# Kernel tuning notes

Hardware: AMD Instinct MI355X
Metric: run time of the kernel (lower is better)

## Reference

```python
import jax, jax.numpy as jnp
import numpy as np

# ---- SLAYER neuron / simulation params (network.yaml equivalents) ----
THETA = 10.0       # spiking threshold
TAU_SR = 10.0      # synaptic (PSP) alpha-kernel time constant
TAU_REF = 1.0      # refractory alpha-kernel time constant
SCALE_REF = 2.0
TS = 1.0           # simulation step
T_SAMPLE = 350     # number of timesteps

B, NIN, NHID, NOUT = 32, 2312, 512, 10


def _alpha_kernel(tau, mult=1.0, eps=0.01):
    # mirrors slayer._calculateAlphaKernel truncation rule
    ks = []
    for t in np.arange(0.0, T_SAMPLE, TS):
        v = mult * t / tau * np.exp(1.0 - t / tau)
        if abs(v) < eps and t > tau:
            break
        ks.append(v)
    return jnp.asarray(np.asarray(ks, dtype=np.float32))

SRM_KERNEL = _alpha_kernel(TAU_SR)                        # truncated PSP kernel
D_REF = float(np.exp(-TS / TAU_REF))                      # geometric decay of refractory alpha kernel
C_REF = float(-SCALE_REF * THETA * np.e * TS / TAU_REF)   # refKernel[j] = C_REF * j * D_REF**j


def psp(x):
    # causal temporal conv with the SRM alpha kernel, scaled by Ts. x: (B, C, T)
    b, c, t = x.shape
    k = SRM_KERNEL.shape[0]
    out = jax.lax.conv_general_dilated(
        x.reshape(b * c, 1, t), SRM_KERNEL[::-1].reshape(1, 1, k),
        window_strides=(1,), padding=[(k - 1, 0)])
    return (out * TS).reshape(b, c, t)


def spike(u_psp):
    # Sequential thresholding with FULL refractory recurrence: a spike at time s
    # adds refKernel[n-s] = C_REF*(n-s)*D_REF**(n-s) to all future potentials.
    # The alpha kernel is realized EXACTLY by a 2-state linear recurrence (x, y):
    #   x[n] = sum_s spk[s] * d^(n-s),  y[n] = sum_s spk[s] * (n-s) * d^(n-s)
    def step(carry, p_t):
        x, y = carry
        y = D_REF * (y + x)
        u = p_t + C_REF * y           # membrane potential after refractory response
        spk = (u >= THETA).astype(p_t.dtype)
        x = D_REF * x + spk
        return (x, y), spk / TS       # SLAYER emits spikes of magnitude 1/Ts
    b, c, _ = u_psp.shape
    init = (jnp.zeros((b, c), u_psp.dtype), jnp.zeros((b, c), u_psp.dtype))
    _, s = jax.lax.scan(step, init, jnp.moveaxis(u_psp, -1, 0))
    return jnp.moveaxis(s, 0, -1)


def setup_inputs() -> dict:
    key = jax.random.key(0)
    k1, k2, k3 = jax.random.split(key, 3)
    spikeInput = (jax.random.uniform(k1, (B, NIN, T_SAMPLE)) < 0.03).astype(jnp.float32) / TS
    W1 = jax.random.normal(k2, (NHID, NIN), jnp.float32) * 0.05
    W2 = jax.random.normal(k3, (NOUT, NHID), jnp.float32) * 0.5
    return {"spikeInput": spikeInput, "W1": W1, "W2": W2}


def reference(spikeInput, W1, W2):
    # fc (1x1x1 conv == per-timestep matmul) -> psp -> spike, twice
    s1 = spike(psp(jnp.einsum('oi,bit->bot', W1, spikeInput)))
    s2 = spike(psp(jnp.einsum('oi,bit->bot', W2, s1)))
    return s2
```

## Files before the change

### kernel.cpp

```cpp
#include <hip/hip_runtime.h>
#include <hip/hip_bf16.h>
#include <math.h>

#define B_    32
#define NIN_  2312
#define NHID_ 512
#define NOUT_ 10
#define T_    350
#define KLEN  77
#define MW    40
#define MAXA2 320

__global__ __launch_bounds__(256) void w1t_k(const float* __restrict__ W,
                                             float* __restrict__ WT) {
  __shared__ float tile[32][33];
  int i0 = blockIdx.x * 32, o0 = blockIdx.y * 32;
  int tx = threadIdx.x, tyb = threadIdx.y;
#pragma unroll
  for (int s = 0; s < 4; ++s) {
    int ty = tyb + s * 8;
    int o = o0 + ty, i = i0 + tx;
    if (i < NIN_) tile[ty][tx] = W[(size_t)o * NIN_ + i];
  }
  __syncthreads();
#pragma unroll
  for (int s = 0; s < 4; ++s) {
    int ty = tyb + s * 8;
    int i = i0 + ty, o = o0 + tx;
    if (i < NIN_) WT[(size_t)i * NHID_ + o] = tile[tx][ty];
  }
}

__global__ __launch_bounds__(256) void inmask_k(const float* __restrict__ X,
                                                unsigned long long* __restrict__ msk) {
  int wave = blockIdx.x * 4 + (threadIdx.x >> 6);
  int lane = threadIdx.x & 63;
  if (wave >= B_ * NIN_) return;
  int b = wave / NIN_, i = wave - b * NIN_;
  const float2* row = (const float2*)(X + (size_t)wave * T_);
  const unsigned long long bit = 1ull << (i & 63);
  unsigned long long* mb = msk + (size_t)b * T_ * MW + (i >> 6);
  for (int p = lane; p < T_ / 2; p += 64) {
    float2 v = row[p];
    if (v.x != 0.f) atomicOr(&mb[(size_t)(2 * p) * MW], bit);
    if (v.y != 0.f) atomicOr(&mb[(size_t)(2 * p + 1) * MW], bit);
  }
}

__global__ __launch_bounds__(256) void accum1_k(const unsigned long long* __restrict__ msk,
                                                const float* __restrict__ WT,
                                                float* __restrict__ Z1) {
  __shared__ unsigned short list[MAXA2];
  __shared__ int ntot;
  int bt = blockIdx.x, tid = threadIdx.x;
  if (tid < 64) {
    unsigned long long w = (tid < 37) ? msk[(size_t)bt * MW + tid] : 0ull;
    int pc = __popcll(w);
    int pre = pc;
#pragma unroll
    for (int d = 1; d < 64; d <<= 1) {
      int o = __shfl_up(pre, d);
      if (tid >= d) pre += o;
    }
    int base = pre - pc;
    if (tid == 63) ntot = pre;
    while (w) {
      int j = __builtin_ctzll(w);
      if (base < MAXA2) list[base] = (unsigned short)(tid * 64 + j);
      ++base;
      w &= w - 1;
    }
  }
  __syncthreads();
  int n = ntot;
  if (n > MAXA2) n = MAXA2;
  float a0 = 0.f, a1 = 0.f;
#pragma unroll 4
  for (int j = 0; j < n; ++j) {
    const float2* w2 = (const float2*)(WT + (size_t)list[j] * NHID_);
    float2 v = w2[tid];
    a0 += v.x;
    a1 += v.y;
  }
  float2* zr = (float2*)(Z1 + (size_t)bt * NHID_);
  zr[tid] = make_float2(a0, a1);
}

__global__ __launch_bounds__(64) void scan1_k(const float* __restrict__ Z1,
                                              unsigned long long* __restrict__ mask) {
  int lane = threadIdx.x;
  int b = blockIdx.x >> 3, g = blockIdx.x & 7;
  int h = g * 64 + lane;
  const double dp   = exp(-0.1);
  const double Ap   = exp(1.0) / 10.0;
  const double D77  = exp(-7.7);
  const float  Dref = (float)exp(-1.0);
  const float  Cref = (float)(-20.0 * exp(1.0));
  double Xc = 0.0, Yc = 0.0, Xd = 0.0, Yd = 0.0;
  float xr = 0.f, yr = 0.f;
  const float* zb = Z1 + (size_t)b * T_ * NHID_ + h;
  unsigned long long* mb = mask + (size_t)b * T_ * 8 + g;
  for (int t0 = 0; t0 < T_; t0 += 16) {
    float z[16], zd[16];
#pragma unroll
    for (int k = 0; k < 16; ++k) {
      int t = t0 + k;
      z[k]  = (t < T_) ? zb[(size_t)t * NHID_] : 0.f;
      zd[k] = (t >= KLEN && t < T_) ? zb[(size_t)(t - KLEN) * NHID_] : 0.f;
    }
#pragma unroll
    for (int k = 0; k < 16; ++k) {
      int t = t0 + k;
      if (t >= T_) break;
      Yc = dp * (Yc + Xc); Xc = dp * Xc + (double)z[k];
      Yd = dp * (Yd + Xd); Xd = dp * Xd + (double)zd[k];
      float p = (float)(Ap * (Yc - D77 * (Yd + 77.0 * Xd)));
      yr = Dref * (yr + xr);
      float u = p + Cref * yr;
      float s = (u >= 10.0f) ? 1.0f : 0.0f;
      xr = Dref * xr + s;
      unsigned long long bw = __ballot(u >= 10.0f);
      if (lane == 0) mb[(size_t)t * 8] = bw;
    }
  }
}

__global__ __launch_bounds__(256) void z2_k(const unsigned long long* __restrict__ mask,
                                            const float* __restrict__ W2,
                                            float* __restrict__ Z2) {
  int wave = blockIdx.x * 4 + (threadIdx.x >> 6);
  int lane = threadIdx.x & 63;
  if (wave >= B_ * T_) return;
  int b = wave / T_, t = wave - b * T_;
  const unsigned long long* m = mask + (size_t)wave * 8;
  if (lane < NOUT_) {
    const float* wr = W2 + (size_t)lane * NHID_;
    float acc = 0.f;
#pragma unroll
    for (int w = 0; w < 8; ++w) {
      unsigned long long mm = m[w];
      while (mm) {
        int j = __builtin_ctzll(mm);
        mm &= mm - 1;
        acc += wr[w * 64 + j];
      }
    }
    Z2[((size_t)b * NOUT_ + lane) * T_ + t] = acc;
  }
}

__global__ __launch_bounds__(64) void scan2_k(const float* __restrict__ Z2,
                                              float* __restrict__ out) {
  int n = blockIdx.x * 64 + threadIdx.x;
  if (n >= B_ * NOUT_) return;
  const double dp   = exp(-0.1);
  const double Ap   = exp(1.0) / 10.0;
  const double D77  = exp(-7.7);
  const float  Dref = (float)exp(-1.0);
  const float  Cref = (float)(-20.0 * exp(1.0));
  double Xc = 0.0, Yc = 0.0, Xd = 0.0, Yd = 0.0;
  float xr = 0.f, yr = 0.f;
  const float* row = Z2 + (size_t)n * T_;
  float* orow = out + (size_t)n * T_;
  float zc = row[0];
  float zdc = 0.f;
  for (int t = 0; t < T_; ++t) {
    float zn  = (t + 1 < T_) ? row[t + 1] : 0.f;
    float zdn = (t + 1 >= KLEN && t + 1 < T_) ? row[t + 1 - KLEN] : 0.f;
    Yc = dp * (Yc + Xc); Xc = dp * Xc + (double)zc;
    Yd = dp * (Yd + Xd); Xd = dp * Xd + (double)zdc;
    float p = (float)(Ap * (Yc - D77 * (Yd + 77.0 * Xd)));
    yr = Dref * (yr + xr);
    float u = p + Cref * yr;
    float s = (u >= 10.0f) ? 1.0f : 0.0f;
    xr = Dref * xr + s;
    orow[t] = s;
    zc = zn; zdc = zdn;
  }
}

extern "C" void kernel_launch(void* const* d_in, const int* in_sizes, int n_in,
                              void* d_out, int out_size, void* d_ws, size_t ws_size,
                              hipStream_t stream) {
  const float* X  = (const float*)d_in[0];
  const float* W1 = (const float*)d_in[1];
  const float* W2 = (const float*)d_in[2];
  float* out = (float*)d_out;

  char* ws = (char*)d_ws;
  size_t off = 0;
  float* W1T = (float*)(ws + off);                 off += (size_t)NIN_ * NHID_ * 4;
  unsigned long long* msk = (unsigned long long*)(ws + off); off += (size_t)B_ * T_ * MW * 8;
  float* Z1 = (float*)(ws + off);                  off += (size_t)B_ * T_ * NHID_ * 4;
  unsigned long long* mask = (unsigned long long*)(ws + off); off += (size_t)B_ * T_ * 8 * 8;
  float* Z2 = (float*)(ws + off);                  off += (size_t)B_ * NOUT_ * T_ * 4;
  if (off > ws_size) return;

  hipMemsetAsync(msk, 0, (size_t)B_ * T_ * MW * 8, stream);

  w1t_k<<<dim3((NIN_ + 31) / 32, NHID_ / 32), dim3(32, 8), 0, stream>>>(W1, W1T);
  inmask_k<<<(B_ * NIN_ + 3) / 4, 256, 0, stream>>>(X, msk);
  accum1_k<<<B_ * T_, 256, 0, stream>>>(msk, W1T, Z1);
  scan1_k<<<B_ * 8, 64, 0, stream>>>(Z1, mask);
  z2_k<<<(B_ * T_ + 3) / 4, 256, 0, stream>>>(mask, W2, Z2);
  scan2_k<<<(B_ * NOUT_ + 63) / 64, 64, 0, stream>>>(Z2, out);
}
```

Baseline: 416.9 us.

## Build input spike masks with ballots, split accumulation over output chunks

The input-mask kernel now assigns each wave a 64-input by 16-timestep tile and builds mask words with ballots and plain stores. This removes the atomicOr traffic and the memset of the mask buffer. The weight accumulation kernel is split into four 64-thread blocks per (batch, time), each covering a 128-column slice, which adds parallelism but recomputes the active-input list in each of the four blocks. The second scan now prefetches its inputs in chunks of 16 timesteps, as the first scan already does.

```diff
diff --git a/kernel.cpp b/kernel.cpp
--- a/kernel.cpp
+++ b/kernel.cpp
@@ -9,6 +9,8 @@
 #define T_    350
 #define KLEN  77
 #define MW    40
+#define NIB   37
+#define NTC   22
 #define MAXA2 320
 
 __global__ __launch_bounds__(256) void w1t_k(const float* __restrict__ W,
@@ -33,57 +35,70 @@
 
 __global__ __launch_bounds__(256) void inmask_k(const float* __restrict__ X,
                                                 unsigned long long* __restrict__ msk) {
-  int wave = blockIdx.x * 4 + (threadIdx.x >> 6);
+  int w = blockIdx.x * 4 + (threadIdx.x >> 6);
   int lane = threadIdx.x & 63;
-  if (wave >= B_ * NIN_) return;
-  int b = wave / NIN_, i = wave - b * NIN_;
-  const float2* row = (const float2*)(X + (size_t)wave * T_);
-  const unsigned long long bit = 1ull << (i & 63);
-  unsigned long long* mb = msk + (size_t)b * T_ * MW + (i >> 6);
-  for (int p = lane; p < T_ / 2; p += 64) {
-    float2 v = row[p];
-    if (v.x != 0.f) atomicOr(&mb[(size_t)(2 * p) * MW], bit);
-    if (v.y != 0.f) atomicOr(&mb[(size_t)(2 * p + 1) * MW], bit);
-  }
-}
-
-__global__ __launch_bounds__(256) void accum1_k(const unsigned long long* __restrict__ msk,
-                                                const float* __restrict__ WT,
-                                                float* __restrict__ Z1) {
+  if (w >= B_ * NIB * NTC) return;
+  int b = w / (NIB * NTC);
+  int rem = w - b * (NIB * NTC);
+  int iblk = rem / NTC, tc = rem - iblk * NTC;
+  int i = iblk * 64 + lane;
+  int t0 = tc * 16;
+  int nk = (t0 + 16 <= T_) ? 16 : (T_ - t0);
+  bool valid = (i < NIN_);
+  const float2* rp = (const float2*)(X + ((size_t)b * NIN_ + (valid ? i : 0)) * T_ + t0);
+  float2 v[8];
+#pragma unroll
+  for (int q = 0; q < 8; ++q) v[q] = make_float2(0.f, 0.f);
+  if (valid) {
+    int nw = nk >> 1;
+    for (int q = 0; q < nw; ++q) v[q] = rp[q];
+  }
+  unsigned long long* mrow = msk + ((size_t)b * T_ + t0) * MW + iblk;
+#pragma unroll
+  for (int k = 0; k < 16; ++k) {
+    if (k >= nk) break;
+    float xv = (k & 1) ? v[k >> 1].y : v[k >> 1].x;
+    unsigned long long bw = __ballot(xv != 0.0f);
+    if (lane == k) mrow[(size_t)k * MW] = bw;
+  }
+}
+
+__global__ __launch_bounds__(64) void accum1_k(const unsigned long long* __restrict__ msk,
+                                               const float* __restrict__ WT,
+                                               float* __restrict__ Z1) {
   __shared__ unsigned short list[MAXA2];
   __shared__ int ntot;
-  int bt = blockIdx.x, tid = threadIdx.x;
-  if (tid < 64) {
-    unsigned long long w = (tid < 37) ? msk[(size_t)bt * MW + tid] : 0ull;
-    int pc = __popcll(w);
-    int pre = pc;
-#pragma unroll
-    for (int d = 1; d < 64; d <<= 1) {
-      int o = __shfl_up(pre, d);
-      if (tid >= d) pre += o;
-    }
-    int base = pre - pc;
-    if (tid == 63) ntot = pre;
-    while (w) {
-      int j = __builtin_ctzll(w);
-      if (base < MAXA2) list[base] = (unsigned short)(tid * 64 + j);
-      ++base;
-      w &= w - 1;
-    }
+  int id = blockIdx.x;
+  int bt = id >> 2, oc = id & 3;
+  int lane = threadIdx.x;
+  unsigned long long wm = (lane < NIB) ? msk[(size_t)bt * MW + lane] : 0ull;
+  int pc = __popcll(wm);
+  int pre = pc;
+#pragma unroll
+  for (int d = 1; d < 64; d <<= 1) {
+    int o = __shfl_up(pre, d);
+    if (lane >= d) pre += o;
+  }
+  int base = pre - pc;
+  if (lane == 63) ntot = pre;
+  while (wm) {
+    int j = __builtin_ctzll(wm);
+    if (base < MAXA2) list[base] = (unsigned short)(lane * 64 + j);
+    ++base;
+    wm &= wm - 1;
   }
   __syncthreads();
   int n = ntot;
   if (n > MAXA2) n = MAXA2;
+  const float2* wbase = (const float2*)WT + (size_t)oc * 64 + lane;
   float a0 = 0.f, a1 = 0.f;
-#pragma unroll 4
+#pragma unroll 8
   for (int j = 0; j < n; ++j) {
-    const float2* w2 = (const float2*)(WT + (size_t)list[j] * NHID_);
-    float2 v = w2[tid];
+    float2 v = wbase[(size_t)list[j] * (NHID_ / 2)];
     a0 += v.x;
     a1 += v.y;
   }
-  float2* zr = (float2*)(Z1 + (size_t)bt * NHID_);
-  zr[tid] = make_float2(a0, a1);
+  ((float2*)(Z1 + (size_t)bt * NHID_))[(size_t)oc * 64 + lane] = make_float2(a0, a1);
 }
 
 __global__ __launch_bounds__(64) void scan1_k(const float* __restrict__ Z1,
@@ -162,20 +177,27 @@
   float xr = 0.f, yr = 0.f;
   const float* row = Z2 + (size_t)n * T_;
   float* orow = out + (size_t)n * T_;
-  float zc = row[0];
-  float zdc = 0.f;
-  for (int t = 0; t < T_; ++t) {
-    float zn  = (t + 1 < T_) ? row[t + 1] : 0.f;
-    float zdn = (t + 1 >= KLEN && t + 1 < T_) ? row[t + 1 - KLEN] : 0.f;
-    Yc = dp * (Yc + Xc); Xc = dp * Xc + (double)zc;
-    Yd = dp * (Yd + Xd); Xd = dp * Xd + (double)zdc;
-    float p = (float)(Ap * (Yc - D77 * (Yd + 77.0 * Xd)));
-    yr = Dref * (yr + xr);
-    float u = p + Cref * yr;
-    float s = (u >= 10.0f) ? 1.0f : 0.0f;
-    xr = Dref * xr + s;
-    orow[t] = s;
-    zc = zn; zdc = zdn;
+  for (int t0 = 0; t0 < T_; t0 += 16) {
+    float z[16], zd[16];
+#pragma unroll
+    for (int k = 0; k < 16; ++k) {
+      int t = t0 + k;
+      z[k]  = (t < T_) ? row[t] : 0.f;
+      zd[k] = (t >= KLEN && t < T_) ? row[t - KLEN] : 0.f;
+    }
+#pragma unroll
+    for (int k = 0; k < 16; ++k) {
+      int t = t0 + k;
+      if (t >= T_) break;
+      Yc = dp * (Yc + Xc); Xc = dp * Xc + (double)z[k];
+      Yd = dp * (Yd + Xd); Xd = dp * Xd + (double)zd[k];
+      float p = (float)(Ap * (Yc - D77 * (Yd + 77.0 * Xd)));
+      yr = Dref * (yr + xr);
+      float u = p + Cref * yr;
+      float s = (u >= 10.0f) ? 1.0f : 0.0f;
+      xr = Dref * xr + s;
+      orow[t] = s;
+    }
   }
 }
 
@@ -196,11 +218,9 @@
   float* Z2 = (float*)(ws + off);                  off += (size_t)B_ * NOUT_ * T_ * 4;
   if (off > ws_size) return;
 
-  hipMemsetAsync(msk, 0, (size_t)B_ * T_ * MW * 8, stream);
-
   w1t_k<<<dim3((NIN_ + 31) / 32, NHID_ / 32), dim3(32, 8), 0, stream>>>(W1, W1T);
-  inmask_k<<<(B_ * NIN_ + 3) / 4, 256, 0, stream>>>(X, msk);
-  accum1_k<<<B_ * T_, 256, 0, stream>>>(msk, W1T, Z1);
+  inmask_k<<<(B_ * NIB * NTC + 3) / 4, 256, 0, stream>>>(X, msk);
+  accum1_k<<<B_ * T_ * 4, 64, 0, stream>>>(msk, W1T, Z1);
   scan1_k<<<B_ * 8, 64, 0, stream>>>(Z1, mask);
   z2_k<<<(B_ * T_ + 3) / 4, 256, 0, stream>>>(mask, W2, Z2);
   scan2_k<<<(B_ * NOUT_ + 63) / 64, 64, 0, stream>>>(Z2, out);
```

Measured after the change: 435.3 us. +4.4%, slower.
